# Kernel optimization log

Measured on AMD Instinct MI355X. Metric: run time of the kernel, lower is better.

The kernel has to match this reference:

```python
import math
import jax, jax.numpy as jnp
import numpy as np

B, T, QDIM, ADIM = 256, 2048, 1024, 128
DC, DK = 8, 21          # dynamic channels / kernel
SC, SK = 8, 21          # static channels / kernel
PL, ALPHA, BETA = 11, 0.1, 0.9


def _betabinom_pmf_flipped(n, a, b, length):
    lg = np.vectorize(math.lgamma)
    k = np.arange(length, dtype=np.float64)
    logp = (lg(n + 1.0) - lg(k + 1.0) - lg(n - k + 1.0)
            + lg(k + a) + lg(n - k + b) - lg(n + a + b)
            - (lg(a) + lg(b) - lg(a + b)))
    return np.exp(logp)[::-1].copy()  # .flip(0) as in the torch buffer


def setup_inputs() -> dict:
    key = jax.random.key(0)
    ks = jax.random.split(key, 10)

    def lin(k, shape, fan_in):
        return (jax.random.normal(k, shape, jnp.float32) / np.sqrt(fan_in)).astype(jnp.float32)

    query = jax.random.normal(ks[0], (B, QDIM), jnp.float32)
    # previous-step alignment: a valid probability distribution over T
    alignment_pre = jax.nn.softmax(2.0 * jax.random.normal(ks[1], (B, T), jnp.float32), axis=1)

    P = jnp.asarray(_betabinom_pmf_flipped(PL - 1, ALPHA, BETA, PL), jnp.float32)
    W_w = lin(ks[2], (ADIM, QDIM), QDIM)
    W_b = jnp.zeros((ADIM,), jnp.float32)
    V_w = lin(ks[3], (DC * DK, ADIM), ADIM)
    F_w = lin(ks[4], (SC, 1, SK), SK)        # Conv1d(1, SC, SK) weight
    U_w = lin(ks[5], (ADIM, SC), SC)
    T_w = lin(ks[6], (ADIM, DC), DC)
    T_b = jnp.zeros((ADIM,), jnp.float32)
    v_w = lin(ks[7], (1, ADIM), ADIM)
    return {"query": query, "alignment_pre": alignment_pre, "P": P,
            "W_w": W_w, "W_b": W_b, "V_w": V_w, "F_w": F_w,
            "U_w": U_w, "T_w": T_w, "T_b": T_b, "v_w": v_w}


def reference(query, alignment_pre, P, W_w, W_b, V_w, F_w, U_w, T_w, T_b, v_w):
    b, t = alignment_pre.shape
    pad = (DK - 1) // 2  # == PL - 1 == 10, shared by all three convs
    x_pad = jnp.pad(alignment_pre, ((0, 0), (pad, pad)))
    # sliding windows (cross-correlation layout): windows[b, t, k] = x_pad[b, t + k]
    windows = jnp.stack([x_pad[:, k:k + t] for k in range(DK)], axis=-1)  # (B, T, DK)

    # prior: causal conv with left pad PL-1 == windows taps 0..PL-1
    p = jnp.log(jnp.clip(jnp.einsum('btk,k->bt', windows[..., :PL], P), 1e-6))

    # per-sample dynamic kernels
    G = jnp.tanh(query @ W_w.T + W_b) @ V_w.T          # (B, DC*DK)
    G = G.reshape(b, DC, DK)
    g = jnp.einsum('btk,bck->btc', windows, G)          # grouped conv, groups=B -> (B, T, DC)

    # static conv over previous alignment
    f = jnp.einsum('btk,ck->btc', windows, F_w[:, 0, :])  # (B, T, SC)

    e = jnp.squeeze(jnp.tanh(f @ U_w.T + g @ T_w.T + T_b) @ v_w.T, -1) + p  # (B, T)
    return jax.nn.softmax(e, axis=1)
```

## Files before the change

### kernel.cpp

```cpp
#include <hip/hip_runtime.h>
#include <hip/hip_bf16.h>

#define Bsz 256
#define Tn 2048
#define QD 1024
#define AD 128
#define DCn 8
#define DKn 21
#define PLn 11
#define GN (DCn * DKn)
#define XS2 24

typedef _Float16 f16x8 __attribute__((ext_vector_type(8)));
typedef float f32x4 __attribute__((ext_vector_type(4)));

#define TWO_LOG2E 2.8853900817779268f

__global__ __launch_bounds__(1024, 4) void dca_kernel(
    const float* __restrict__ query, const float* __restrict__ align,
    const float* __restrict__ P, const float* __restrict__ W_w,
    const float* __restrict__ W_b, const float* __restrict__ V_w,
    const float* __restrict__ F_w, const float* __restrict__ U_w,
    const float* __restrict__ T_w, const float* __restrict__ T_b,
    const float* __restrict__ v_w, float* __restrict__ out)
{
    __shared__ _Float16 al16[Tn + 44];
    __shared__ float    pcb[Tn];
    __shared__ float    sden[Tn];
    __shared__ _Float16 Xw[16 * 2 * 16 * XS2];
    __shared__ float    h_lds[AD];
    __shared__ float    G_lds[GN];
    __shared__ float    red[16];
    __shared__ float    bc;

    const int b    = blockIdx.x;
    const int tid  = threadIdx.x;
    const int lane = tid & 63;
    const int wid  = tid >> 6;
    const int l15  = lane & 15;
    const int quad = lane >> 4;

    for (int i = tid; i < Tn + 44; i += 1024) {
        int s = i - 10;
        float v = (s >= 0 && s < Tn) ? align[b * Tn + s] : 0.f;
        al16[i] = (_Float16)v;
    }

    {
        const float4* q4 = (const float4*)(query + b * QD);
        float4 q0 = q4[lane];
        float4 q1 = q4[64 + lane];
        float4 q2 = q4[128 + lane];
        float4 q3 = q4[192 + lane];
        #pragma unroll 2
        for (int i = 0; i < 8; ++i) {
            int a = wid * 8 + i;
            const float4* w4 = (const float4*)(W_w + a * QD);
            float4 x0 = w4[lane];
            float4 x1 = w4[64 + lane];
            float4 x2 = w4[128 + lane];
            float4 x3 = w4[192 + lane];
            float accA = 0.f, accB = 0.f;
            accA = fmaf(q0.x, x0.x, fmaf(q0.y, x0.y, fmaf(q0.z, x0.z, fmaf(q0.w, x0.w, accA))));
            accB = fmaf(q1.x, x1.x, fmaf(q1.y, x1.y, fmaf(q1.z, x1.z, fmaf(q1.w, x1.w, accB))));
            accA = fmaf(q2.x, x2.x, fmaf(q2.y, x2.y, fmaf(q2.z, x2.z, fmaf(q2.w, x2.w, accA))));
            accB = fmaf(q3.x, x3.x, fmaf(q3.y, x3.y, fmaf(q3.z, x3.z, fmaf(q3.w, x3.w, accB))));
            float acc = accA + accB;
            #pragma unroll
            for (int off = 32; off; off >>= 1) acc += __shfl_xor(acc, off);
            if (lane == 0) h_lds[a] = tanhf(acc + W_b[a]);
        }
    }
    __syncthreads();

    if (tid < GN) {
        float g = 0.f;
        #pragma unroll 4
        for (int i = 0; i < AD; ++i) g = fmaf(h_lds[i], V_w[tid * AD + i], g);
        G_lds[tid] = g;
    }

    const int t0w = wid * 128;
    #pragma unroll
    for (int tt = 0; tt < 2; ++tt) {
        int t = t0w + tt * 64 + lane;
        float pr = 0.f;
        #pragma unroll
        for (int k = 0; k < PLn; ++k) pr = fmaf((float)al16[t + k], P[k], pr);
        pcb[t] = fmaxf(pr, 1e-6f);
    }
    __syncthreads();

    f16x8 Bc = {};
    #pragma unroll
    for (int j = 0; j < 8; ++j) {
        int k = quad * 8 + j;
        float wv = 0.f;
        if (k < DKn) wv = (l15 < 8) ? F_w[l15 * DKn + k]
                                    : G_lds[(l15 - 8) * DKn + k];
        Bc[j] = (_Float16)wv;
    }

    f16x8 Bf[8];
    #pragma unroll
    for (int n = 0; n < 8; ++n) {
        int a = n * 16 + l15;
        f16x8 bf = {};
        if (quad < 2) {
            const float* src = (quad == 0) ? (U_w + a * 8) : (T_w + a * 8);
            float4 lo = ((const float4*)src)[0];
            float4 hi = ((const float4*)src)[1];
            bf[0] = (_Float16)(TWO_LOG2E * lo.x); bf[1] = (_Float16)(TWO_LOG2E * lo.y);
            bf[2] = (_Float16)(TWO_LOG2E * lo.z); bf[3] = (_Float16)(TWO_LOG2E * lo.w);
            bf[4] = (_Float16)(TWO_LOG2E * hi.x); bf[5] = (_Float16)(TWO_LOG2E * hi.y);
            bf[6] = (_Float16)(TWO_LOG2E * hi.z); bf[7] = (_Float16)(TWO_LOG2E * hi.w);
        } else if (quad == 2) {
            bf[0] = (_Float16)(TWO_LOG2E * T_b[a]);
        }
        Bf[n] = bf;
    }

    f32x4 vnq[8];
    float vsum = 0.f;
    #pragma unroll
    for (int n = 0; n < 8; ++n) {
        f32x4 vq = *(const f32x4*)(v_w + n * 16 + quad * 4);
        vsum += vq[0] + vq[1] + vq[2] + vq[3];
        vq[0] *= -2.f; vq[1] *= -2.f; vq[2] *= -2.f; vq[3] *= -2.f;
        vnq[n] = vq;
    }
    vsum += __shfl_xor(vsum, 16);
    vsum += __shfl_xor(vsum, 32);

    _Float16* Xp0 = &Xw[wid * 2 * 16 * XS2];
    _Float16* Xp1 = Xp0 + 16 * XS2;
    float wsum = 0.f;

    #pragma unroll 1
    for (int m = 0; m < 8; m += 2) {
        const int ta  = t0w + m * 16;
        const int tb_ = ta + 16;

        f16x8 Ac0, Ac1;
        #pragma unroll
        for (int j = 0; j < 8; ++j) {
            Ac0[j] = al16[ta  + l15 + quad * 8 + j];
            Ac1[j] = al16[tb_ + l15 + quad * 8 + j];
        }
        f32x4 z = {};
        f32x4 X0 = __builtin_amdgcn_mfma_f32_16x16x32_f16(Ac0, Bc, z, 0, 0, 0);
        f32x4 X1 = __builtin_amdgcn_mfma_f32_16x16x32_f16(Ac1, Bc, z, 0, 0, 0);

        #pragma unroll
        for (int r = 0; r < 4; ++r) {
            Xp0[(quad * 4 + r) * XS2 + l15] = (_Float16)X0[r];
            Xp1[(quad * 4 + r) * XS2 + l15] = (_Float16)X1[r];
        }
        __asm__ __volatile__("" ::: "memory");

        f16x8 B20 = {}, B21 = {};
        if (quad < 2) {
            B20 = *(const f16x8*)&Xp0[l15 * XS2 + quad * 8];
            B21 = *(const f16x8*)&Xp1[l15 * XS2 + quad * 8];
        } else if (quad == 2) {
            B20[0] = (_Float16)1.f;
            B21[0] = (_Float16)1.f;
        }

        float es0 = 0.f, es1 = 0.f;
        #pragma unroll
        for (int n = 0; n < 8; ++n) {
            f32x4 z2 = {};
            f32x4 d0 = __builtin_amdgcn_mfma_f32_16x16x32_f16(Bf[n], B20, z2, 0, 0, 0);
            f32x4 d1 = __builtin_amdgcn_mfma_f32_16x16x32_f16(Bf[n], B21, z2, 0, 0, 0);
            #pragma unroll
            for (int r = 0; r < 4; ++r) {
                float qa = __builtin_amdgcn_exp2f(d0[r]);
                float qb = __builtin_amdgcn_exp2f(d1[r]);
                float ra = __builtin_amdgcn_rcpf(qa + 1.f);
                float rb = __builtin_amdgcn_rcpf(qb + 1.f);
                es0 = fmaf(vnq[n][r], ra, es0);
                es1 = fmaf(vnq[n][r], rb, es1);
            }
        }
        es0 += __shfl_xor(es0, 16);
        es0 += __shfl_xor(es0, 32);
        es1 += __shfl_xor(es1, 16);
        es1 += __shfl_xor(es1, 32);

        if (lane < 16) {
            int tA = ta  + lane;
            int tB = tb_ + lane;
            float svA = pcb[tA] * __expf(es0 + vsum);
            float svB = pcb[tB] * __expf(es1 + vsum);
            sden[tA] = svA;
            sden[tB] = svB;
            wsum += svA + svB;
        }
    }

    __syncthreads();
    #pragma unroll
    for (int off = 32; off; off >>= 1) wsum += __shfl_xor(wsum, off);
    if (lane == 0) red[wid] = wsum;
    __syncthreads();
    if (wid == 0) {
        float ss = (lane < 16) ? red[lane] : 0.f;
        #pragma unroll
        for (int off = 8; off; off >>= 1) ss += __shfl_xor(ss, off);
        if (lane == 0) bc = ss;
    }
    __syncthreads();
    const float inv = 1.f / bc;
    out[b * Tn + tid]        = sden[tid] * inv;
    out[b * Tn + tid + 1024] = sden[tid + 1024] * inv;
}

extern "C" void kernel_launch(void* const* d_in, const int* in_sizes, int n_in,
                              void* d_out, int out_size, void* d_ws, size_t ws_size,
                              hipStream_t stream) {
    const float* query = (const float*)d_in[0];
    const float* align = (const float*)d_in[1];
    const float* P     = (const float*)d_in[2];
    const float* W_w   = (const float*)d_in[3];
    const float* W_b   = (const float*)d_in[4];
    const float* V_w   = (const float*)d_in[5];
    const float* F_w   = (const float*)d_in[6];
    const float* U_w   = (const float*)d_in[7];
    const float* T_w   = (const float*)d_in[8];
    const float* T_b   = (const float*)d_in[9];
    const float* v_w   = (const float*)d_in[10];
    float* out = (float*)d_out;

    dca_kernel<<<Bsz, 1024, 0, stream>>>(query, align, P, W_w, W_b, V_w,
                                         F_w, U_w, T_w, T_b, v_w, out);
}
```

Before: 106.0 us.

## Split fused kernel into G-projection, segmented main, and normalization kernels

```diff
diff --git a/kernel.cpp b/kernel.cpp
--- a/kernel.cpp
+++ b/kernel.cpp
@@ -10,86 +10,108 @@
 #define PLn 11
 #define GN (DCn * DKn)
 #define XS2 24
+#define SEGT 256
+#define NSEG (Tn / SEGT)
 
 typedef _Float16 f16x8 __attribute__((ext_vector_type(8)));
 typedef float f32x4 __attribute__((ext_vector_type(4)));
 
 #define TWO_LOG2E 2.8853900817779268f
 
-__global__ __launch_bounds__(1024, 4) void dca_kernel(
-    const float* __restrict__ query, const float* __restrict__ align,
-    const float* __restrict__ P, const float* __restrict__ W_w,
+__global__ __launch_bounds__(512) void g_kernel(
+    const float* __restrict__ query, const float* __restrict__ W_w,
     const float* __restrict__ W_b, const float* __restrict__ V_w,
+    float* __restrict__ G_ws, float* __restrict__ rowsum)
+{
+    __shared__ float h_lds[AD];
+    const int b    = blockIdx.x;
+    const int tid  = threadIdx.x;
+    const int w    = tid >> 6;
+    const int lane = tid & 63;
+
+    if (tid == 0) rowsum[b] = 0.f;
+
+    const float4* q4 = (const float4*)(query + b * QD);
+    float4 q0 = q4[lane];
+    float4 q1 = q4[64 + lane];
+    float4 q2 = q4[128 + lane];
+    float4 q3 = q4[192 + lane];
+
+    #pragma unroll 2
+    for (int i = 0; i < 16; ++i) {
+        int a = w * 16 + i;
+        const float4* w4 = (const float4*)(W_w + a * QD);
+        float4 x0 = w4[lane];
+        float4 x1 = w4[64 + lane];
+        float4 x2 = w4[128 + lane];
+        float4 x3 = w4[192 + lane];
+        float accA = 0.f, accB = 0.f;
+        accA = fmaf(q0.x, x0.x, fmaf(q0.y, x0.y, fmaf(q0.z, x0.z, fmaf(q0.w, x0.w, accA))));
+        accB = fmaf(q1.x, x1.x, fmaf(q1.y, x1.y, fmaf(q1.z, x1.z, fmaf(q1.w, x1.w, accB))));
+        accA = fmaf(q2.x, x2.x, fmaf(q2.y, x2.y, fmaf(q2.z, x2.z, fmaf(q2.w, x2.w, accA))));
+        accB = fmaf(q3.x, x3.x, fmaf(q3.y, x3.y, fmaf(q3.z, x3.z, fmaf(q3.w, x3.w, accB))));
+        float acc = accA + accB;
+        #pragma unroll
+        for (int off = 32; off; off >>= 1) acc += __shfl_xor(acc, off);
+        if (lane == 0) h_lds[a] = tanhf(acc + W_b[a]);
+    }
+    __syncthreads();
+
+    for (int r = w; r < GN; r += 8) {
+        float acc = fmaf(h_lds[lane], V_w[r * AD + lane],
+                         h_lds[64 + lane] * V_w[r * AD + 64 + lane]);
+        #pragma unroll
+        for (int off = 32; off; off >>= 1) acc += __shfl_xor(acc, off);
+        if (lane == 0) G_ws[b * GN + r] = acc;
+    }
+}
+
+__global__ __launch_bounds__(256, 5) void dca_main(
+    const float* __restrict__ align, const float* __restrict__ P,
     const float* __restrict__ F_w, const float* __restrict__ U_w,
     const float* __restrict__ T_w, const float* __restrict__ T_b,
-    const float* __restrict__ v_w, float* __restrict__ out)
+    const float* __restrict__ v_w, const float* __restrict__ G_ws,
+    float* __restrict__ out, float* __restrict__ rowsum)
 {
-    __shared__ _Float16 al16[Tn + 44];
-    __shared__ float    pcb[Tn];
-    __shared__ float    sden[Tn];
-    __shared__ _Float16 Xw[16 * 2 * 16 * XS2];
-    __shared__ float    h_lds[AD];
-    __shared__ float    G_lds[GN];
-    __shared__ float    red[16];
-    __shared__ float    bc;
-
-    const int b    = blockIdx.x;
+    __shared__ _Float16 al16[SEGT + 44];
+    __shared__ float    pcb[SEGT];
+    __shared__ _Float16 Xw[4 * 2 * 16 * XS2];
+    __shared__ float    vlds[AD];
+    __shared__ float    vsum_lds;
+    __shared__ float    red[4];
+
+    const int bid  = blockIdx.x;
+    const int b    = bid >> 3;
+    const int seg  = bid & (NSEG - 1);
+    const int t0s  = seg * SEGT;
     const int tid  = threadIdx.x;
     const int lane = tid & 63;
     const int wid  = tid >> 6;
     const int l15  = lane & 15;
     const int quad = lane >> 4;
 
-    for (int i = tid; i < Tn + 44; i += 1024) {
-        int s = i - 10;
+    for (int i = tid; i < SEGT + 44; i += 256) {
+        int s = t0s + i - 10;
         float v = (s >= 0 && s < Tn) ? align[b * Tn + s] : 0.f;
         al16[i] = (_Float16)v;
     }
+    if (tid < 32) {
+        float4 v4 = ((const float4*)v_w)[tid];
+        float s4 = v4.x + v4.y + v4.z + v4.w;
+        #pragma unroll
+        for (int off = 16; off; off >>= 1) s4 += __shfl_xor(s4, off);
+        if (tid == 0) vsum_lds = s4;
+        ((float4*)vlds)[tid] = make_float4(-2.f * v4.x, -2.f * v4.y,
+                                           -2.f * v4.z, -2.f * v4.w);
+    }
+    __syncthreads();
 
     {
-        const float4* q4 = (const float4*)(query + b * QD);
-        float4 q0 = q4[lane];
-        float4 q1 = q4[64 + lane];
-        float4 q2 = q4[128 + lane];
-        float4 q3 = q4[192 + lane];
-        #pragma unroll 2
-        for (int i = 0; i < 8; ++i) {
-            int a = wid * 8 + i;
-            const float4* w4 = (const float4*)(W_w + a * QD);
-            float4 x0 = w4[lane];
-            float4 x1 = w4[64 + lane];
-            float4 x2 = w4[128 + lane];
-            float4 x3 = w4[192 + lane];
-            float accA = 0.f, accB = 0.f;
-            accA = fmaf(q0.x, x0.x, fmaf(q0.y, x0.y, fmaf(q0.z, x0.z, fmaf(q0.w, x0.w, accA))));
-            accB = fmaf(q1.x, x1.x, fmaf(q1.y, x1.y, fmaf(q1.z, x1.z, fmaf(q1.w, x1.w, accB))));
-            accA = fmaf(q2.x, x2.x, fmaf(q2.y, x2.y, fmaf(q2.z, x2.z, fmaf(q2.w, x2.w, accA))));
-            accB = fmaf(q3.x, x3.x, fmaf(q3.y, x3.y, fmaf(q3.z, x3.z, fmaf(q3.w, x3.w, accB))));
-            float acc = accA + accB;
-            #pragma unroll
-            for (int off = 32; off; off >>= 1) acc += __shfl_xor(acc, off);
-            if (lane == 0) h_lds[a] = tanhf(acc + W_b[a]);
-        }
-    }
-    __syncthreads();
-
-    if (tid < GN) {
-        float g = 0.f;
-        #pragma unroll 4
-        for (int i = 0; i < AD; ++i) g = fmaf(h_lds[i], V_w[tid * AD + i], g);
-        G_lds[tid] = g;
-    }
-
-    const int t0w = wid * 128;
-    #pragma unroll
-    for (int tt = 0; tt < 2; ++tt) {
-        int t = t0w + tt * 64 + lane;
         float pr = 0.f;
         #pragma unroll
-        for (int k = 0; k < PLn; ++k) pr = fmaf((float)al16[t + k], P[k], pr);
-        pcb[t] = fmaxf(pr, 1e-6f);
-    }
-    __syncthreads();
+        for (int k = 0; k < PLn; ++k) pr = fmaf((float)al16[tid + k], P[k], pr);
+        pcb[tid] = fmaxf(pr, 1e-6f);
+    }
 
     f16x8 Bc = {};
     #pragma unroll
@@ -97,7 +119,7 @@
         int k = quad * 8 + j;
         float wv = 0.f;
         if (k < DKn) wv = (l15 < 8) ? F_w[l15 * DKn + k]
-                                    : G_lds[(l15 - 8) * DKn + k];
+                                    : G_ws[b * GN + (l15 - 8) * DKn + k];
         Bc[j] = (_Float16)wv;
     }
 
@@ -119,33 +141,24 @@
         }
         Bf[n] = bf;
     }
-
-    f32x4 vnq[8];
-    float vsum = 0.f;
-    #pragma unroll
-    for (int n = 0; n < 8; ++n) {
-        f32x4 vq = *(const f32x4*)(v_w + n * 16 + quad * 4);
-        vsum += vq[0] + vq[1] + vq[2] + vq[3];
-        vq[0] *= -2.f; vq[1] *= -2.f; vq[2] *= -2.f; vq[3] *= -2.f;
-        vnq[n] = vq;
-    }
-    vsum += __shfl_xor(vsum, 16);
-    vsum += __shfl_xor(vsum, 32);
-
+    const float vsum = vsum_lds;
+
+    const int tw = wid * 64;
     _Float16* Xp0 = &Xw[wid * 2 * 16 * XS2];
     _Float16* Xp1 = Xp0 + 16 * XS2;
+    float* orow = out + b * Tn + t0s;
     float wsum = 0.f;
 
     #pragma unroll 1
-    for (int m = 0; m < 8; m += 2) {
-        const int ta  = t0w + m * 16;
-        const int tb_ = ta + 16;
+    for (int m = 0; m < 2; ++m) {
+        const int tlA = tw + m * 32;
+        const int tlB = tlA + 16;
 
         f16x8 Ac0, Ac1;
         #pragma unroll
         for (int j = 0; j < 8; ++j) {
-            Ac0[j] = al16[ta  + l15 + quad * 8 + j];
-            Ac1[j] = al16[tb_ + l15 + quad * 8 + j];
+            Ac0[j] = al16[tlA + l15 + quad * 8 + j];
+            Ac1[j] = al16[tlB + l15 + quad * 8 + j];
         }
         f32x4 z = {};
         f32x4 X0 = __builtin_amdgcn_mfma_f32_16x16x32_f16(Ac0, Bc, z, 0, 0, 0);
@@ -170,6 +183,7 @@
         float es0 = 0.f, es1 = 0.f;
         #pragma unroll
         for (int n = 0; n < 8; ++n) {
+            f32x4 vq = *(const f32x4*)&vlds[n * 16 + quad * 4];
             f32x4 z2 = {};
             f32x4 d0 = __builtin_amdgcn_mfma_f32_16x16x32_f16(Bf[n], B20, z2, 0, 0, 0);
             f32x4 d1 = __builtin_amdgcn_mfma_f32_16x16x32_f16(Bf[n], B21, z2, 0, 0, 0);
@@ -179,8 +193,8 @@
                 float qb = __builtin_amdgcn_exp2f(d1[r]);
                 float ra = __builtin_amdgcn_rcpf(qa + 1.f);
                 float rb = __builtin_amdgcn_rcpf(qb + 1.f);
-                es0 = fmaf(vnq[n][r], ra, es0);
-                es1 = fmaf(vnq[n][r], rb, es1);
+                es0 = fmaf(vq[r], ra, es0);
+                es1 = fmaf(vq[r], rb, es1);
             }
         }
         es0 += __shfl_xor(es0, 16);
@@ -189,31 +203,35 @@
         es1 += __shfl_xor(es1, 32);
 
         if (lane < 16) {
-            int tA = ta  + lane;
-            int tB = tb_ + lane;
-            float svA = pcb[tA] * __expf(es0 + vsum);
-            float svB = pcb[tB] * __expf(es1 + vsum);
-            sden[tA] = svA;
-            sden[tB] = svB;
+            float svA = pcb[tlA + lane] * __expf(es0 + vsum);
+            float svB = pcb[tlB + lane] * __expf(es1 + vsum);
+            orow[tlA + lane] = svA;
+            orow[tlB + lane] = svB;
             wsum += svA + svB;
         }
     }
 
-    __syncthreads();
     #pragma unroll
     for (int off = 32; off; off >>= 1) wsum += __shfl_xor(wsum, off);
     if (lane == 0) red[wid] = wsum;
     __syncthreads();
-    if (wid == 0) {
-        float ss = (lane < 16) ? red[lane] : 0.f;
-        #pragma unroll
-        for (int off = 8; off; off >>= 1) ss += __shfl_xor(ss, off);
-        if (lane == 0) bc = ss;
-    }
-    __syncthreads();
-    const float inv = 1.f / bc;
-    out[b * Tn + tid]        = sden[tid] * inv;
-    out[b * Tn + tid + 1024] = sden[tid + 1024] * inv;
+    if (tid == 0)
+        atomicAdd(rowsum + b, red[0] + red[1] + red[2] + red[3]);
+}
+
+__global__ __launch_bounds__(256) void norm_kernel(
+    float* __restrict__ out, const float* __restrict__ rowsum)
+{
+    const int b = blockIdx.x;
+    const float inv = 1.f / rowsum[b];
+    float4* o = (float4*)(out + b * Tn);
+    #pragma unroll
+    for (int i = 0; i < Tn / 4 / 256; ++i) {
+        int idx = i * 256 + threadIdx.x;
+        float4 v = o[idx];
+        v.x *= inv; v.y *= inv; v.z *= inv; v.w *= inv;
+        o[idx] = v;
+    }
 }
 
 extern "C" void kernel_launch(void* const* d_in, const int* in_sizes, int n_in,
@@ -230,8 +248,12 @@
     const float* T_w   = (const float*)d_in[8];
     const float* T_b   = (const float*)d_in[9];
     const float* v_w   = (const float*)d_in[10];
-    float* out = (float*)d_out;
-
-    dca_kernel<<<Bsz, 1024, 0, stream>>>(query, align, P, W_w, W_b, V_w,
-                                         F_w, U_w, T_w, T_b, v_w, out);
-}
+    float* out    = (float*)d_out;
+    float* G_ws   = (float*)d_ws;
+    float* rowsum = G_ws + Bsz * GN;
+
+    g_kernel<<<Bsz, 512, 0, stream>>>(query, W_w, W_b, V_w, G_ws, rowsum);
+    dca_main<<<Bsz * NSEG, 256, 0, stream>>>(align, P, F_w, U_w, T_w, T_b,
+                                             v_w, G_ws, out, rowsum);
+    norm_kernel<<<Bsz, 256, 0, stream>>>(out, rowsum);
+}
```

Measured after the change: 126.3 us. 1.19x slower.
